# Optimization experiments

Measured on AMD Instinct MI355X. Metric: run time of the kernel, lower is better.

## Reference

```python
import jax, jax.numpy as jnp
import numpy as np

NTR = 4
DTR = 0.0
DELTA = 3


def _get_edges(im, ntr, dtr):
    # im: [N, H, W] float
    N, H, W = im.shape
    d = DELTA
    im_b = jnp.ones((N, H + 2 * d, W + 2 * d), im.dtype).at[:, d:d + H, d:d + W].set(im)
    r = lambda a, s: jnp.roll(a, s, axis=(1, 2))
    diff_11 = r(im_b, (1, 1)) - im_b
    diff_nn11 = r(im_b, (-1, -1)) - im_b
    diff_01 = r(im_b, (0, 1)) - im_b
    diff_n01 = r(im_b, (0, -1)) - im_b
    diff_10 = r(im_b, (1, 0)) - im_b
    diff_n10 = r(im_b, (-1, 0)) - im_b
    diff_n11 = r(im_b, (-1, 1)) - im_b
    diff_1n1 = r(im_b, (1, -1)) - im_b
    gt = lambda a, b: (a > b).astype(jnp.int32)
    thr = lambda dd: jnp.abs(dd) * (jnp.abs(dd) > dtr).astype(im.dtype)

    ad_10 = thr(diff_10)
    c10 = (gt(ad_10, jnp.abs(diff_01)) + gt(ad_10, jnp.abs(diff_n01)) + gt(ad_10, jnp.abs(diff_n10))
           + gt(ad_10, jnp.abs(r(diff_01, (1, 0)))) + gt(ad_10, jnp.abs(r(diff_n01, (1, 0)))) + gt(ad_10, jnp.abs(r(diff_01, (1, 0)))))
    e10 = (c10 > ntr) & (diff_10 > 0)
    e10n = (c10 > ntr) & (diff_10 < 0)

    ad_01 = thr(diff_01)
    c01 = (gt(ad_01, jnp.abs(diff_10)) + gt(ad_01, jnp.abs(diff_n10)) + gt(ad_01, jnp.abs(diff_n01))
           + gt(ad_01, jnp.abs(r(diff_10, (0, 1)))) + gt(ad_01, jnp.abs(r(diff_n10, (0, 1)))) + gt(ad_01, jnp.abs(r(diff_01, (0, 1)))))
    e01 = (c01 > ntr) & (diff_01 > 0)
    e01n = (c01 > ntr) & (diff_01 < 0)

    ad_11 = thr(diff_11)
    c11 = (gt(ad_11, jnp.abs(diff_n11)) + gt(ad_11, jnp.abs(diff_1n1)) + gt(ad_11, jnp.abs(diff_nn11))
           + gt(ad_11, jnp.abs(r(diff_n11, (1, 1)))) + gt(ad_11, jnp.abs(r(diff_1n1, (1, 1)))) + gt(ad_11, jnp.abs(r(diff_11, (1, 1)))))
    e11 = (c11 > ntr) & (diff_11 > 0)
    e11n = (c11 > ntr) & (diff_11 < 0)

    ad_n11 = thr(diff_n11)
    cn11 = (gt(ad_n11, jnp.abs(diff_11)) + gt(ad_n11, jnp.abs(diff_1n1)) + gt(ad_n11, jnp.abs(diff_nn11))
            + gt(ad_n11, jnp.abs(r(diff_11, (-1, 1)))) + gt(ad_n11, jnp.abs(r(diff_n11, (-1, 1)))) + gt(ad_n11, jnp.abs(r(diff_n11, (-1, 1)))))
    en11 = (cn11 > ntr) & (diff_n11 > 0)
    en11n = (cn11 > ntr) & (diff_n11 < 0)

    f = lambda b: jnp.where(b, jnp.array(1, im.dtype), jnp.array(0, im.dtype))
    edges = jnp.zeros((N, 8, H, W), im.dtype)
    edges = edges.at[:, 0, 2:H, 0:W].set(f(e10[:, d + 2:d + H, d:d + W]))
    edges = edges.at[:, 1, 0:H - 2, 0:W].set(f(e10n[:, d:d + H - 2, d:d + W]))
    edges = edges.at[:, 2, 0:H, 2:W].set(f(e01[:, d:d + H, d + 2:d + W]))
    edges = edges.at[:, 3, 0:H, 0:W - 2].set(f(e01n[:, d:d + H, d:d + W - 2]))
    edges = edges.at[:, 4, 2:H, 2:W].set(f(e11[:, d + 2:d + H, d + 2:d + W]))
    edges = edges.at[:, 5, 0:H - 2, 0:W - 2].set(f(e11n[:, d:d + H - 2, d:d + W - 2]))
    edges = edges.at[:, 6, 0:H - 2, 2:W].set(f(en11[:, d:d + H - 2, d + 2:d + W]))
    edges = edges.at[:, 7, 2:H, 0:W - 2].set(f(en11n[:, d + 2:d + H, d:d + W - 2]))
    return edges


def setup_inputs() -> dict:
    key = jax.random.key(0)
    x = jax.random.normal(key, (16, 3, 512, 512), dtype=jnp.float32)
    return {"x": x}


def reference(x):
    B, C, H, W = x.shape
    # pre_edges concatenates per-channel get_edges along dim 1 -> [B, 8*C, H, W]
    im = x.reshape(B * C, H, W)
    edges = _get_edges(im, NTR, DTR)  # [B*C, 8, H, W]
    return edges.reshape(B, C * 8, H, W)
```

## Files before the change

### kernel.cpp

```cpp
#include <hip/hip_runtime.h>


#define IMG_H 512
#define IMG_W 512

typedef float float4v __attribute__((ext_vector_type(4)));
typedef float float2v __attribute__((ext_vector_type(2)));

__device__ __forceinline__ void edge_core(
    float pcc, float pmm, float pm0, float pmp,
    float p0m, float p0p, float ppm, float pp0, float ppp,
    float p0mm, float pmm0, float pmmmm, float pppmm,
    float o[8])
{
    float d10   = pm0 - pcc;
    float dn10  = pp0 - pcc;
    float d01   = p0m - pcc;
    float dn01  = p0p - pcc;
    float d11   = pmm - pcc;
    float dnn11 = ppp - pcc;
    float dn11  = ppm - pcc;
    float d1n1  = pmp - pcc;

    float a10 = fabsf(d10),  an10  = fabsf(dn10);
    float a01 = fabsf(d01),  an01  = fabsf(dn01);
    float a11 = fabsf(d11),  ann11 = fabsf(dnn11);
    float an11 = fabsf(dn11), a1n1 = fabsf(d1n1);

    int c10 = (int)(a10 > a01) + (int)(a10 > an01) + (int)(a10 > an10)
            + 2 * (int)(a10 > fabsf(pmm - pm0))
            + (int)(a10 > fabsf(pmp - pm0));

    int c01 = (int)(a01 > a10) + (int)(a01 > an10) + (int)(a01 > an01)
            + (int)(a01 > fabsf(pmm - p0m))
            + (int)(a01 > fabsf(ppm - p0m))
            + (int)(a01 > fabsf(p0mm - p0m));

    int c11 = (int)(a11 > an11) + (int)(a11 > a1n1) + (int)(a11 > ann11)
            + (int)(a11 > fabsf(p0mm - pmm))
            + (int)(a11 > fabsf(pmm0 - pmm))
            + (int)(a11 > fabsf(pmmmm - pmm));

    int cn11 = (int)(an11 > a11) + (int)(an11 > a1n1) + (int)(an11 > ann11)
             + (int)(an11 > fabsf(p0mm - ppm))
             + 2 * (int)(an11 > fabsf(pppmm - ppm));

    o[0] = (c10 > 4 && d10 > 0.f) ? 1.f : 0.f;
    o[1] = (c10 > 4 && d10 < 0.f) ? 1.f : 0.f;
    o[2] = (c01 > 4 && d01 > 0.f) ? 1.f : 0.f;
    o[3] = (c01 > 4 && d01 < 0.f) ? 1.f : 0.f;
    o[4] = (c11 > 4 && d11 > 0.f) ? 1.f : 0.f;
    o[5] = (c11 > 4 && d11 < 0.f) ? 1.f : 0.f;
    o[6] = (cn11 > 4 && dn11 > 0.f) ? 1.f : 0.f;
    o[7] = (cn11 > 4 && dn11 < 0.f) ? 1.f : 0.f;
}

__global__ __launch_bounds__(256) void edge_kernel(const float* __restrict__ in,
                                                   float* __restrict__ out,
                                                   int nimg) {
    int idx = blockIdx.x * blockDim.x + threadIdx.x;
    int wq = idx & (IMG_W / 4 - 1);
    int h = (idx >> 7) & (IMG_H - 1);
    int n = idx >> 16;
    if (n >= nimg) return;
    int w0 = wq * 4;

    const float* img = in + (size_t)n * IMG_H * IMG_W;

    const float* rM2 = img + max(h - 2, 0) * IMG_W;
    const float* rM1 = img + max(h - 1, 0) * IMG_W;
    const float* R0  = img + h * IMG_W;
    const float* rP1 = img + min(h + 1, IMG_H - 1) * IMG_W;
    const float* rP2 = img + min(h + 2, IMG_H - 1) * IMG_W;

    bool vm2 = (h >= 2), vm1 = (h >= 1);
    bool vp1 = (h <= IMG_H - 2), vp2 = (h <= IMG_H - 3);
    bool vl = (w0 != 0);
    bool vr = (w0 != IMG_W - 4);
    int cl2 = max(w0 - 2, 0);
    int cl1 = max(w0 - 1, 0);
    int cr4 = min(w0 + 4, IMG_W - 1);

    float4v m_m2 = *(const float4v*)(rM2 + w0);
    float4v m_m1 = *(const float4v*)(rM1 + w0);
    float4v m_0  = *(const float4v*)(R0  + w0);
    float4v m_p1 = *(const float4v*)(rP1 + w0);
    float2v m_p2 = *(const float2v*)(rP2 + w0);

    float rm2[6], rm1[6], r0[7], rp1[6], rp2[4];

    rm2[0] = (vm2 && vl) ? rM2[cl2] : 1.0f;
    rm2[1] = (vm2 && vl) ? rM2[cl1] : 1.0f;
#pragma unroll
    for (int j = 0; j < 4; ++j) rm2[j + 2] = vm2 ? m_m2[j] : 1.0f;

    rm1[0] = (vm1 && vl) ? rM1[cl1] : 1.0f;
#pragma unroll
    for (int j = 0; j < 4; ++j) rm1[j + 1] = vm1 ? m_m1[j] : 1.0f;
    rm1[5] = (vm1 && vr) ? rM1[cr4] : 1.0f;

    r0[0] = vl ? R0[cl2] : 1.0f;
    r0[1] = vl ? R0[cl1] : 1.0f;
#pragma unroll
    for (int j = 0; j < 4; ++j) r0[j + 2] = m_0[j];
    r0[6] = vr ? R0[cr4] : 1.0f;

    rp1[0] = (vp1 && vl) ? rP1[cl1] : 1.0f;
#pragma unroll
    for (int j = 0; j < 4; ++j) rp1[j + 1] = vp1 ? m_p1[j] : 1.0f;
    rp1[5] = (vp1 && vr) ? rP1[cr4] : 1.0f;

    rp2[0] = (vp2 && vl) ? rP2[cl2] : 1.0f;
    rp2[1] = (vp2 && vl) ? rP2[cl1] : 1.0f;
    rp2[2] = vp2 ? m_p2[0] : 1.0f;
    rp2[3] = vp2 ? m_p2[1] : 1.0f;

    float4v ov[8];
    bool hge2 = (h >= 2), hlt = (h < IMG_H - 2);

#pragma unroll
    for (int i = 0; i < 4; ++i) {
        float o[8];
        edge_core(r0[i + 2],
                  rm1[i], rm1[i + 1], rm1[i + 2],
                  r0[i + 1], r0[i + 3],
                  rp1[i], rp1[i + 1], rp1[i + 2],
                  r0[i],
                  rm2[i + 2],
                  rm2[i],
                  rp2[i],
                  o);
        int w = w0 + i;
        bool wge2 = (w >= 2), wlt = (w < IMG_W - 2);
        ov[0][i] = hge2           ? o[0] : 0.f;
        ov[1][i] = hlt            ? o[1] : 0.f;
        ov[2][i] = wge2           ? o[2] : 0.f;
        ov[3][i] = wlt            ? o[3] : 0.f;
        ov[4][i] = (hge2 && wge2) ? o[4] : 0.f;
        ov[5][i] = (hlt && wlt)   ? o[5] : 0.f;
        ov[6][i] = (hlt && wge2)  ? o[6] : 0.f;
        ov[7][i] = (hge2 && wlt)  ? o[7] : 0.f;
    }

    const size_t cs = (size_t)IMG_H * IMG_W;
    float* obase = out + ((size_t)n * 8) * cs + (size_t)h * IMG_W + w0;
#pragma unroll
    for (int k = 0; k < 8; ++k) {
        __builtin_nontemporal_store(ov[k], (float4v*)(obase + (size_t)k * cs));
    }
}

extern "C" void kernel_launch(void* const* d_in, const int* in_sizes, int n_in,
                              void* d_out, int out_size, void* d_ws, size_t ws_size,
                              hipStream_t stream) {
    const float* x = (const float*)d_in[0];
    float* out = (float*)d_out;
    int nimg = in_sizes[0] / (IMG_H * IMG_W);
    long long total = (long long)nimg * IMG_H * (IMG_W / 4);
    int block = 256;
    int grid = (int)((total + block - 1) / block);
    edge_kernel<<<grid, block, 0, stream>>>(x, out, nimg);
}
```

Measured before the change: 82.78 us.

## Split edge kernel into bit-pack pass and coalesced expand pass

Splits the work into two kernels. The first computes the 8 edge flags for 4 pixels and packs them into one 32-bit word in the workspace. The second expands those bits into float outputs, with each thread writing one contiguous float4 in output order, so writes are fully coalesced instead of strided across 8 channel planes. This costs an extra kernel launch, a small workspace round trip and the loss of the nontemporal stores.

After: 121.7 us. +47.0%, slower.

```diff
diff --git a/kernel.cpp b/kernel.cpp
--- a/kernel.cpp
+++ b/kernel.cpp
@@ -7,25 +7,20 @@
 typedef float float4v __attribute__((ext_vector_type(4)));
 typedef float float2v __attribute__((ext_vector_type(2)));
 
-__device__ __forceinline__ void edge_core(
+__device__ __forceinline__ unsigned edge_mask(
     float pcc, float pmm, float pm0, float pmp,
     float p0m, float p0p, float ppm, float pp0, float ppp,
-    float p0mm, float pmm0, float pmmmm, float pppmm,
-    float o[8])
+    float p0mm, float pmm0, float pmmmm, float pppmm)
 {
     float d10   = pm0 - pcc;
-    float dn10  = pp0 - pcc;
     float d01   = p0m - pcc;
-    float dn01  = p0p - pcc;
     float d11   = pmm - pcc;
-    float dnn11 = ppp - pcc;
     float dn11  = ppm - pcc;
-    float d1n1  = pmp - pcc;
 
-    float a10 = fabsf(d10),  an10  = fabsf(dn10);
-    float a01 = fabsf(d01),  an01  = fabsf(dn01);
-    float a11 = fabsf(d11),  ann11 = fabsf(dnn11);
-    float an11 = fabsf(dn11), a1n1 = fabsf(d1n1);
+    float a10 = fabsf(d10),  an10  = fabsf(pp0 - pcc);
+    float a01 = fabsf(d01),  an01  = fabsf(p0p - pcc);
+    float a11 = fabsf(d11),  ann11 = fabsf(ppp - pcc);
+    float an11 = fabsf(dn11), a1n1 = fabsf(pmp - pcc);
 
     int c10 = (int)(a10 > a01) + (int)(a10 > an01) + (int)(a10 > an10)
             + 2 * (int)(a10 > fabsf(pmm - pm0))
@@ -45,24 +40,25 @@
              + (int)(an11 > fabsf(p0mm - ppm))
              + 2 * (int)(an11 > fabsf(pppmm - ppm));
 
-    o[0] = (c10 > 4 && d10 > 0.f) ? 1.f : 0.f;
-    o[1] = (c10 > 4 && d10 < 0.f) ? 1.f : 0.f;
-    o[2] = (c01 > 4 && d01 > 0.f) ? 1.f : 0.f;
-    o[3] = (c01 > 4 && d01 < 0.f) ? 1.f : 0.f;
-    o[4] = (c11 > 4 && d11 > 0.f) ? 1.f : 0.f;
-    o[5] = (c11 > 4 && d11 < 0.f) ? 1.f : 0.f;
-    o[6] = (cn11 > 4 && dn11 > 0.f) ? 1.f : 0.f;
-    o[7] = (cn11 > 4 && dn11 < 0.f) ? 1.f : 0.f;
+    unsigned m = 0;
+    m |= (c10  > 4 && d10  > 0.f) ? 1u   : 0u;
+    m |= (c10  > 4 && d10  < 0.f) ? 2u   : 0u;
+    m |= (c01  > 4 && d01  > 0.f) ? 4u   : 0u;
+    m |= (c01  > 4 && d01  < 0.f) ? 8u   : 0u;
+    m |= (c11  > 4 && d11  > 0.f) ? 16u  : 0u;
+    m |= (c11  > 4 && d11  < 0.f) ? 32u  : 0u;
+    m |= (cn11 > 4 && dn11 > 0.f) ? 64u  : 0u;
+    m |= (cn11 > 4 && dn11 < 0.f) ? 128u : 0u;
+    return m;
 }
 
-__global__ __launch_bounds__(256) void edge_kernel(const float* __restrict__ in,
-                                                   float* __restrict__ out,
-                                                   int nimg) {
+__global__ __launch_bounds__(256) void edge_pack_kernel(
+    const float* __restrict__ in, unsigned* __restrict__ ws)
+{
     int idx = blockIdx.x * blockDim.x + threadIdx.x;
     int wq = idx & (IMG_W / 4 - 1);
     int h = (idx >> 7) & (IMG_H - 1);
     int n = idx >> 16;
-    if (n >= nimg) return;
     int w0 = wq * 4;
 
     const float* img = in + (size_t)n * IMG_H * IMG_W;
@@ -115,39 +111,52 @@
     rp2[2] = vp2 ? m_p2[0] : 1.0f;
     rp2[3] = vp2 ? m_p2[1] : 1.0f;
 
-    float4v ov[8];
     bool hge2 = (h >= 2), hlt = (h < IMG_H - 2);
+    unsigned gh = (hge2 ? 0x11u : 0u)
+                | (hlt  ? 0x62u : 0u)
+                | (hge2 ? 0x80u : 0u)
+                | (hlt  ? 0x20u : 0u);
+    gh = (hge2 ? 0x91u : 0u) | (hlt ? 0x62u : 0u) | 0x0Cu;
 
+    unsigned pk = 0;
 #pragma unroll
     for (int i = 0; i < 4; ++i) {
-        float o[8];
-        edge_core(r0[i + 2],
-                  rm1[i], rm1[i + 1], rm1[i + 2],
-                  r0[i + 1], r0[i + 3],
-                  rp1[i], rp1[i + 1], rp1[i + 2],
-                  r0[i],
-                  rm2[i + 2],
-                  rm2[i],
-                  rp2[i],
-                  o);
+        unsigned m = edge_mask(
+            r0[i + 2],
+            rm1[i], rm1[i + 1], rm1[i + 2],
+            r0[i + 1], r0[i + 3],
+            rp1[i], rp1[i + 1], rp1[i + 2],
+            r0[i],
+            rm2[i + 2],
+            rm2[i],
+            rp2[i]);
         int w = w0 + i;
         bool wge2 = (w >= 2), wlt = (w < IMG_W - 2);
-        ov[0][i] = hge2           ? o[0] : 0.f;
-        ov[1][i] = hlt            ? o[1] : 0.f;
-        ov[2][i] = wge2           ? o[2] : 0.f;
-        ov[3][i] = wlt            ? o[3] : 0.f;
-        ov[4][i] = (hge2 && wge2) ? o[4] : 0.f;
-        ov[5][i] = (hlt && wlt)   ? o[5] : 0.f;
-        ov[6][i] = (hlt && wge2)  ? o[6] : 0.f;
-        ov[7][i] = (hge2 && wlt)  ? o[7] : 0.f;
+        unsigned gw = 0x03u | (wge2 ? 0x54u : 0u) | (wlt ? 0xA8u : 0u);
+        m &= gh & gw;
+        pk |= m << (8 * i);
     }
+    ws[idx] = pk;
+}
 
-    const size_t cs = (size_t)IMG_H * IMG_W;
-    float* obase = out + ((size_t)n * 8) * cs + (size_t)h * IMG_W + w0;
-#pragma unroll
-    for (int k = 0; k < 8; ++k) {
-        __builtin_nontemporal_store(ov[k], (float4v*)(obase + (size_t)k * cs));
-    }
+__global__ __launch_bounds__(256) void edge_expand_kernel(
+    const unsigned* __restrict__ ws, float* __restrict__ out)
+{
+    int f = blockIdx.x * blockDim.x + threadIdx.x;
+    int q = f & 127;
+    int h = (f >> 7) & (IMG_H - 1);
+    int p = (f >> 16) & 7;
+    int n = f >> 19;
+
+    unsigned pk = ws[((n << 9) | h) << 7 | q];
+
+    float4v v;
+    v[0] = ((pk >> p)        & 1u) ? 1.f : 0.f;
+    v[1] = ((pk >> (8 + p))  & 1u) ? 1.f : 0.f;
+    v[2] = ((pk >> (16 + p)) & 1u) ? 1.f : 0.f;
+    v[3] = ((pk >> (24 + p)) & 1u) ? 1.f : 0.f;
+
+    ((float4v*)out)[f] = v;
 }
 
 extern "C" void kernel_launch(void* const* d_in, const int* in_sizes, int n_in,
@@ -155,9 +164,10 @@
                               hipStream_t stream) {
     const float* x = (const float*)d_in[0];
     float* out = (float*)d_out;
+    unsigned* ws = (unsigned*)d_ws;
     int nimg = in_sizes[0] / (IMG_H * IMG_W);
-    long long total = (long long)nimg * IMG_H * (IMG_W / 4);
-    int block = 256;
-    int grid = (int)((total + block - 1) / block);
-    edge_kernel<<<grid, block, 0, stream>>>(x, out, nimg);
+    int grid1 = nimg * IMG_H * (IMG_W / 4) / 256;
+    edge_pack_kernel<<<grid1, 256, 0, stream>>>(x, ws);
+    int grid2 = out_size / 4 / 256;
+    edge_expand_kernel<<<grid2, 256, 0, stream>>>(ws, out);
 }
```
